# Optimization experiments

Measured on AMD Instinct MI355X. Metric: run time of the kernel, lower is better.

The kernel has to match this reference:

```python
import jax, jax.numpy as jnp
import numpy as np
import math

T, N, P, H, E, S, R = 64, 1024, 256, 256, 512, 16, 16

def _sincos(n, d):
    pos = np.arange(n)[:, None].astype(np.float32)
    div = np.exp(np.arange(0, d, 2).astype(np.float32) * -(math.log(10000.0) / d))
    pe = np.zeros((n, d), np.float32)
    pe[:, 0::2] = np.sin(pos * div)
    pe[:, 1::2] = np.cos(pos * div)
    return jnp.asarray(pe)

def setup_inputs():
    key = jax.random.key(0)
    ks = iter(jax.random.split(key, 40))
    def w(shape, s=0.05):
        return jax.random.normal(next(ks), shape, jnp.float32) * s
    adj_seq = (jax.random.uniform(next(ks), (T, N, N)) < 0.05).astype(jnp.float32)
    return dict(
        adj_seq=adj_seq,
        pos_emb=_sincos(N, P),
        g1_Wm=w((P, H)), g1_bm=jnp.zeros((H,), jnp.float32),
        g1_Wq=w((H, H)), g1_Wk=w((H, H)), g1_gb=jnp.asarray(-1.0, jnp.float32),
        g1_Wu=w((P + H, H)), g1_bu=jnp.zeros((H,), jnp.float32),
        g1_lg=jnp.ones((H,), jnp.float32), g1_lb=jnp.zeros((H,), jnp.float32),
        g2_Wm=w((H, H)), g2_bm=jnp.zeros((H,), jnp.float32),
        g2_Wu=w((2 * H, H)), g2_bu=jnp.zeros((H,), jnp.float32),
        g2_lg=jnp.ones((H,), jnp.float32), g2_lb=jnp.zeros((H,), jnp.float32),
        m_lg=jnp.ones((H,), jnp.float32), m_lb=jnp.zeros((H,), jnp.float32),
        m_Win=w((H, 2 * E)), m_bin=jnp.zeros((2 * E,), jnp.float32),
        m_Wdelta=w((E, R)), m_bdelta=jnp.zeros((R,), jnp.float32),
        m_Wdt=w((R, E)), m_bdt=jnp.zeros((E,), jnp.float32),
        m_WB=w((E, S)), m_bB=jnp.zeros((S,), jnp.float32),
        m_WC=w((E, S)), m_bC=jnp.zeros((S,), jnp.float32),
        m_Alog=-jnp.exp(w((E, S), 0.1)),
        m_D=jnp.zeros((E,), jnp.float32),
        m_Wout=w((E, H)), m_bout=jnp.zeros((H,), jnp.float32),
    )

def _ln(x, g, b):
    mu = x.mean(-1, keepdims=True)
    v = ((x - mu) ** 2).mean(-1, keepdims=True)
    return (x - mu) / jnp.sqrt(v + 1e-5) * g + b

def reference(adj_seq, pos_emb, g1_Wm, g1_bm, g1_Wq, g1_Wk, g1_gb, g1_Wu, g1_bu,
              g1_lg, g1_lb, g2_Wm, g2_bm, g2_Wu, g2_bu, g2_lg, g2_lb,
              m_lg, m_lb, m_Win, m_bin, m_Wdelta, m_bdelta, m_Wdt, m_bdt,
              m_WB, m_bB, m_WC, m_bC, m_Alog, m_D, m_Wout, m_bout):
    scale = math.sqrt(H) * max(1.0, 1e-6)  # sqrt(d) * gate_temperature

    def encode(adj):  # adj: [N,N]
        msgs = pos_emb @ g1_Wm + g1_bm                 # [N,H]
        q = msgs @ g1_Wq
        k = msgs @ g1_Wk
        gates = jax.nn.sigmoid(q @ k.T / scale + g1_gb)
        agg = (gates * adj) @ msgs                     # gated aggregation
        x = _ln(jax.nn.relu(jnp.concatenate([pos_emb, agg], -1) @ g1_Wu + g1_bu), g1_lg, g1_lb)
        msgs2 = x @ g2_Wm + g2_bm
        agg2 = adj @ msgs2                             # ungated layer 2
        x = _ln(jax.nn.relu(jnp.concatenate([x, agg2], -1) @ g2_Wu + g2_bu), g2_lg, g2_lb)
        return x                                       # [N,H]

    seq = jax.vmap(encode)(adj_seq)                    # [T,N,H]
    x = seq.transpose(1, 0, 2)                         # [N,T,H] node-batched sequences

    # --- MambaBlock ---
    res = x
    xn = _ln(x, m_lg, m_lb)
    xp = xn @ m_Win + m_bin
    u, gate = jnp.split(xp, 2, axis=-1)                # [N,T,E] each
    u = jax.nn.silu(u)
    delta = jax.nn.softplus((u @ m_Wdelta + m_bdelta) @ m_Wdt + m_bdt)  # [N,T,E]
    Bm = u @ m_WB + m_bB                               # [N,T,S]
    Cm = u @ m_WC + m_bC                               # [N,T,S]
    A = -jnp.exp(m_Alog)                               # [E,S]

    def step(h, inp):
        u_t, d_t, B_t, C_t = inp                       # [N,E],[N,E],[N,S],[N,S]
        Ad = jnp.exp(d_t[:, :, None] * A[None])        # [N,E,S]
        h = Ad * h + d_t[:, :, None] * B_t[:, None, :] * u_t[:, :, None]
        y = jnp.einsum('ns,nes->ne', C_t, h)
        return h, y

    h0 = jnp.zeros((N, E, S), x.dtype)
    _, ys = jax.lax.scan(step, h0, (u.transpose(1, 0, 2), delta.transpose(1, 0, 2),
                                    Bm.transpose(1, 0, 2), Cm.transpose(1, 0, 2)))
    y = ys.transpose(1, 0, 2)                          # [N,T,E]
    y = (y + u * m_D) * jax.nn.silu(gate)
    out = y @ m_Wout + m_bout + res                    # [N,T,H]
    return out.transpose(1, 0, 2)                      # [T,N,H]
```

## Files before the change

kernel.cpp:

```cpp
#include <hip/hip_runtime.h>
#include <hip/hip_bf16.h>

typedef __hip_bfloat16 bf16;
typedef __attribute__((ext_vector_type(8))) short s16x8;
typedef __attribute__((ext_vector_type(4))) short s16x4;
typedef __attribute__((ext_vector_type(4))) float f32x4;

#define TT 64
#define NN_ 1024
#define EE 512

__device__ __forceinline__ float toF(float v) { return v; }
__device__ __forceinline__ float toF(bf16 v) { return __bfloat162float(v); }
__device__ __forceinline__ bf16 f2b(float v) { return __float2bfloat16(v); }

#if __has_builtin(__builtin_amdgcn_exp2f)
#define EXP2F(x) __builtin_amdgcn_exp2f(x)
#else
#define EXP2F(x) exp2f(x)
#endif
#if __has_builtin(__builtin_amdgcn_logf)
#define LOG2F(x) __builtin_amdgcn_logf(x)
#else
#define LOG2F(x) log2f(x)
#endif

enum { EPI_F32 = 0, EPI_SIG_F32 = 1, EPI_SIG_B16 = 2 };
enum { E_LN1 = 0, E_BF16 = 1, E_LN2 = 2, E_SILU = 3, E_OUT = 4, E_TRI = 5, E_BF16T = 6 };

template <bool TRANSB, int EPI>
__global__ __launch_bounds__(256) void gemm_k(
    const float* __restrict__ A, const float* __restrict__ B,
    float* __restrict__ outF, const float* __restrict__ bias,
    const float* __restrict__ sbeta, float alpha,
    int M, int Nn, int K, int lda, int ldb)
{
    __shared__ float As[16][68];
    __shared__ float Bs[16][68];
    const int tid = threadIdx.x;
    const int tx = tid & 15, ty = tid >> 4;
    const int m0 = blockIdx.x * 64, n0 = blockIdx.y * 64;
    float acc[4][4] = {};

    for (int k0 = 0; k0 < K; k0 += 16) {
        {
            int row = tid >> 2, kk0 = (tid & 3) * 4, grow = m0 + row;
#pragma unroll
            for (int j = 0; j < 4; j++) {
                int kk = kk0 + j, gk = k0 + kk;
                As[kk][row] = (grow < M) ? A[(size_t)grow * lda + gk] : 0.f;
            }
        }
        if (!TRANSB) {
            int kk = tid >> 4, c0 = (tid & 15) * 4;
#pragma unroll
            for (int j = 0; j < 4; j++) {
                int col = c0 + j, gn = n0 + col;
                Bs[kk][col] = (gn < Nn) ? B[(size_t)(k0 + kk) * ldb + gn] : 0.f;
            }
        } else {
            int col = tid >> 2, kk0 = (tid & 3) * 4, gn = n0 + col;
#pragma unroll
            for (int j = 0; j < 4; j++) {
                int kk = kk0 + j;
                Bs[kk][col] = (gn < Nn) ? B[(size_t)gn * ldb + (k0 + kk)] : 0.f;
            }
        }
        __syncthreads();
#pragma unroll
        for (int kk = 0; kk < 16; kk++) {
            float a[4], b[4];
#pragma unroll
            for (int i = 0; i < 4; i++) a[i] = As[kk][ty * 4 + i];
#pragma unroll
            for (int j = 0; j < 4; j++) b[j] = Bs[kk][tx * 4 + j];
#pragma unroll
            for (int i = 0; i < 4; i++)
#pragma unroll
                for (int j = 0; j < 4; j++)
                    acc[i][j] = fmaf(a[i], b[j], acc[i][j]);
        }
        __syncthreads();
    }

    float gb = (EPI != EPI_F32 && sbeta) ? sbeta[0] : 0.f;
#pragma unroll
    for (int i = 0; i < 4; i++) {
        int row = m0 + ty * 4 + i;
        if (row >= M) continue;
#pragma unroll
        for (int j = 0; j < 4; j++) {
            int col = n0 + tx * 4 + j;
            if (col >= Nn) continue;
            float v = acc[i][j];
            if (EPI == EPI_F32) {
                if (bias) v += bias[col];
                outF[(size_t)row * Nn + col] = v;
            } else if (EPI == EPI_SIG_F32) {
                v = v * alpha + gb;
                outF[(size_t)row * Nn + col] = 1.f / (1.f + __expf(-v));
            } else {
                v = v * alpha + gb;
                ((bf16*)outF)[(size_t)row * Nn + col] = f2b(1.f / (1.f + __expf(-v)));
            }
        }
    }
}

template <int BM, int BN, bool CAT, int EPI>
__global__ __launch_bounds__(256) void mfma_k(
    const bf16* __restrict__ A1, const bf16* __restrict__ A2, unsigned rowmask,
    const bf16* __restrict__ BT, const float* __restrict__ bias,
    float* __restrict__ outF,
    bf16* __restrict__ outB, bf16* __restrict__ outB2,
    const float* __restrict__ g1, const float* __restrict__ b1,
    const float* __restrict__ g2, const float* __restrict__ b2,
    const bf16* __restrict__ resid,
    int M, int K)
{
    constexpr bool LN = (EPI == E_LN1 || EPI == E_LN2);
    constexpr int STAGE_B = (BM * 32 + BN * 32) * 2;
    constexpr int TRB = (EPI == E_BF16T) ? (64 * 268 * 2) : 0;
    constexpr int SB = LN ? (64 * 260 * 4) : (STAGE_B > TRB ? STAGE_B : TRB);
    __shared__ __align__(16) char smem[SB];
    short* As = (short*)smem;
    short* Bs = As + BM * 32;
    float* Cs = (float*)smem;

    const int tid = threadIdx.x;
    const int wid = tid >> 6, lane = tid & 63;
    const int wr = (BN == 256) ? 0 : wid;
    const int wc = (BN == 256) ? wid : 0;
    const int m0 = blockIdx.x * BM, n0 = blockIdx.y * BN;
    const int srow = tid >> 2;
    const int skoff = (tid & 3) * 8;

    f32x4 acc[4][4] = {};
    s16x8 pa[BM / 64], pbv[BN / 64];

    auto LOADT = [&](int k0) {
#pragma unroll
        for (int c = 0; c < BM / 64; c++) {
            int r = c * 64 + srow;
            int gr = m0 + r;
            const bf16* p;
            if (CAT) {
                int gk = k0 + skoff;
                p = (gk < 256) ? (A1 + (size_t)(gr & rowmask) * 256 + gk)
                               : (A2 + (size_t)gr * 256 + (gk - 256));
            } else {
                p = A1 + (size_t)gr * K + k0 + skoff;
            }
            pa[c] = *(const s16x8*)p;
        }
#pragma unroll
        for (int c = 0; c < BN / 64; c++) {
            int r = c * 64 + srow;
            pbv[c] = *(const s16x8*)(BT + (size_t)(n0 + r) * K + k0 + skoff);
        }
    };

    LOADT(0);
#pragma unroll 1
    for (int k0 = 0; k0 < K; k0 += 32) {
#pragma unroll
        for (int c = 0; c < BM / 64; c++)
            *(s16x8*)&As[(c * 64 + srow) * 32 + skoff] = pa[c];
#pragma unroll
        for (int c = 0; c < BN / 64; c++)
            *(s16x8*)&Bs[(c * 64 + srow) * 32 + skoff] = pbv[c];
        __syncthreads();
        if (k0 + 32 < K) LOADT(k0 + 32);
        s16x8 af[4], bf[4];
#pragma unroll
        for (int mi = 0; mi < 4; mi++)
            af[mi] = *(s16x8*)&As[(wr * 64 + mi * 16 + (lane & 15)) * 32 + (lane >> 4) * 8];
#pragma unroll
        for (int ni = 0; ni < 4; ni++)
            bf[ni] = *(s16x8*)&Bs[(wc * 64 + ni * 16 + (lane & 15)) * 32 + (lane >> 4) * 8];
#pragma unroll
        for (int mi = 0; mi < 4; mi++)
#pragma unroll
            for (int ni = 0; ni < 4; ni++)
                acc[mi][ni] = __builtin_amdgcn_mfma_f32_16x16x32_bf16(
                    af[mi], bf[ni], acc[mi][ni], 0, 0, 0);
        __syncthreads();
    }

    if (EPI == E_SILU) {
#pragma unroll
        for (int mi = 0; mi < 4; mi++)
#pragma unroll
            for (int ni = 0; ni < 4; ni++)
#pragma unroll
                for (int r = 0; r < 4; r++) {
                    int row = m0 + wr * 64 + mi * 16 + (lane >> 4) * 4 + r;
                    int col = n0 + wc * 64 + ni * 16 + (lane & 15);
                    float v = acc[mi][ni][r] + bias[col];
                    float s = v / (1.f + __expf(-v));
                    if (col < EE) outB[(size_t)row * EE + col] = f2b(s);
                    else          outB2[(size_t)row * EE + (col - EE)] = f2b(s);
                }
    } else if (EPI == E_BF16) {
#pragma unroll
        for (int mi = 0; mi < 4; mi++)
#pragma unroll
            for (int ni = 0; ni < 4; ni++)
#pragma unroll
                for (int r = 0; r < 4; r++) {
                    int row = m0 + wr * 64 + mi * 16 + (lane >> 4) * 4 + r;
                    int col = n0 + wc * 64 + ni * 16 + (lane & 15);
                    outB[(size_t)row * 256 + col] = f2b(acc[mi][ni][r] + bias[col]);
                }
    } else if (EPI == E_BF16T) {
        short* Ts = (short*)smem;
#pragma unroll
        for (int mi = 0; mi < 4; mi++)
#pragma unroll
            for (int ni = 0; ni < 4; ni++)
#pragma unroll
                for (int r = 0; r < 4; r++) {
                    int rl = mi * 16 + (lane >> 4) * 4 + r;
                    int cl = wc * 64 + ni * 16 + (lane & 15);
                    union { bf16 b; short s; } u;
                    u.b = f2b(acc[mi][ni][r] + bias[cl]);
                    Ts[rl * 268 + cl] = u.s;
                }
        __syncthreads();
        const int col = tid;
        size_t dbase = (((size_t)(m0 >> 10)) * 256 + col) * 1024 + (m0 & 1023);
#pragma unroll
        for (int j0 = 0; j0 < 64; j0 += 8) {
            s16x8 v;
#pragma unroll
            for (int i = 0; i < 8; i++) v[i] = Ts[(j0 + i) * 268 + col];
            *(s16x8*)&outB[dbase + j0] = v;
        }
    } else if (EPI == E_OUT) {
#pragma unroll
        for (int mi = 0; mi < 4; mi++)
#pragma unroll
            for (int ni = 0; ni < 4; ni++)
#pragma unroll
                for (int r = 0; r < 4; r++) {
                    int row = m0 + wr * 64 + mi * 16 + (lane >> 4) * 4 + r;
                    int col = n0 + wc * 64 + ni * 16 + (lane & 15);
                    float v = acc[mi][ni][r] + bias[col] + toF(resid[(size_t)row * 256 + col]);
                    int t = row & 63, n = row >> 6;
                    outF[((size_t)t * NN_ + n) * 256 + col] = v;
                }
    } else if (EPI == E_TRI) {
#pragma unroll
        for (int mi = 0; mi < 4; mi++)
#pragma unroll
            for (int ni = 0; ni < 4; ni++)
#pragma unroll
                for (int r = 0; r < 4; r++) {
                    int row = m0 + wid * 64 + mi * 16 + (lane >> 4) * 4 + r;
                    int col = ni * 16 + (lane & 15);
                    if (col < 48) {
                        float v = acc[mi][ni][r] + bias[col];
                        outF[(size_t)row * 48 + col] = v;
                    }
                }
    } else {
#pragma unroll
        for (int mi = 0; mi < 4; mi++)
#pragma unroll
            for (int ni = 0; ni < 4; ni++)
#pragma unroll
                for (int r = 0; r < 4; r++) {
                    int rl = mi * 16 + (lane >> 4) * 4 + r;
                    int cl = wc * 64 + ni * 16 + (lane & 15);
                    Cs[rl * 260 + cl] = fmaxf(acc[mi][ni][r] + bias[cl], 0.f);
                }
        __syncthreads();
        float g1v[4], b1v[4], g2v[4], b2v[4];
#pragma unroll
        for (int i = 0; i < 4; i++) {
            g1v[i] = g1[lane * 4 + i];
            b1v[i] = b1[lane * 4 + i];
            if (EPI == E_LN2) { g2v[i] = g2[lane * 4 + i]; b2v[i] = b2[lane * 4 + i]; }
        }
        for (int rr = 0; rr < 16; rr++) {
            int rl = wid * 16 + rr;
            int grow = m0 + rl;
            float x[4];
#pragma unroll
            for (int i = 0; i < 4; i++) x[i] = Cs[rl * 260 + lane * 4 + i];
            float s = x[0] + x[1] + x[2] + x[3];
#pragma unroll
            for (int o = 1; o < 64; o <<= 1) s += __shfl_xor(s, o, 64);
            float mu = s * (1.f / 256.f);
            float d[4], ss = 0.f;
#pragma unroll
            for (int i = 0; i < 4; i++) { d[i] = x[i] - mu; ss = fmaf(d[i], d[i], ss); }
#pragma unroll
            for (int o = 1; o < 64; o <<= 1) ss += __shfl_xor(ss, o, 64);
            float inv = rsqrtf(fmaxf(ss * (1.f / 256.f), 0.f) + 1e-5f);
            float y[4];
#pragma unroll
            for (int i = 0; i < 4; i++) y[i] = d[i] * inv * g1v[i] + b1v[i];
            if (EPI == E_LN1) {
                __align__(8) bf16 pk[4];
#pragma unroll
                for (int i = 0; i < 4; i++) pk[i] = f2b(y[i]);
                *(s16x4*)&outB[(size_t)grow * 256 + lane * 4] = *(s16x4*)pk;
            } else {
                int trow = (grow & 1023) * 64 + (grow >> 10);
                __align__(8) bf16 pk[4];
#pragma unroll
                for (int i = 0; i < 4; i++) pk[i] = f2b(y[i]);
                *(s16x4*)&outB[(size_t)trow * 256 + lane * 4] = *(s16x4*)pk;
                float s2 = y[0] + y[1] + y[2] + y[3];
#pragma unroll
                for (int o = 1; o < 64; o <<= 1) s2 += __shfl_xor(s2, o, 64);
                float mu2 = s2 * (1.f / 256.f);
                float d2[4], ss2 = 0.f;
#pragma unroll
                for (int i = 0; i < 4; i++) { d2[i] = y[i] - mu2; ss2 = fmaf(d2[i], d2[i], ss2); }
#pragma unroll
                for (int o = 1; o < 64; o <<= 1) ss2 += __shfl_xor(ss2, o, 64);
                float inv2 = rsqrtf(fmaxf(ss2 * (1.f / 256.f), 0.f) + 1e-5f);
                __align__(8) bf16 pk2[4];
#pragma unroll
                for (int i = 0; i < 4; i++) pk2[i] = f2b(d2[i] * inv2 * g2v[i] + b2v[i]);
                *(s16x4*)&outB2[(size_t)trow * 256 + lane * 4] = *(s16x4*)pk2;
            }
        }
    }
}

__global__ __launch_bounds__(256) void packadj_k(
    const float4* __restrict__ adj4, unsigned int* __restrict__ bits32)
{
    const size_t nwords = (size_t)TT * NN_ * NN_ / 32;
    const size_t stride = (size_t)gridDim.x * 256;
    for (size_t w = (size_t)blockIdx.x * 256 + threadIdx.x; w < nwords; w += stride) {
        const float4* __restrict__ p = adj4 + w * 8;
        float4 v[8];
#pragma unroll
        for (int i = 0; i < 8; i++) v[i] = p[i];
        unsigned int m = 0;
#pragma unroll
        for (int i = 0; i < 8; i++) {
            m |= (v[i].x != 0.f ? 1u : 0u) << (4 * i);
            m |= (v[i].y != 0.f ? 2u : 0u) << (4 * i);
            m |= (v[i].z != 0.f ? 4u : 0u) << (4 * i);
            m |= (v[i].w != 0.f ? 8u : 0u) << (4 * i);
        }
        bits32[w] = m;
    }
}

template <bool GATED>
__global__ __launch_bounds__(256, 2) void aggmm_k(
    const unsigned char* __restrict__ adjbits, const bf16* __restrict__ gatesb,
    const bf16* __restrict__ BTsrc, bf16* __restrict__ out)
{
    __shared__ __align__(16) short As[128 * 40];
    __shared__ __align__(16) short Bs[256 * 40];
    const int tid = threadIdx.x;
    const int wid = tid >> 6, lane = tid & 63;
    const int wr = wid & 1;
    const int wc = wid >> 1;
    const int bx = blockIdx.x;
    const int t = bx >> 3, n0 = (bx & 7) * 128;
    const int srow = tid >> 2;
    const int skoff = (tid & 3) * 8;

    const unsigned char* __restrict__ abB =
        adjbits + ((size_t)t * 1024 + n0) * 128 + (tid & 3);
    const bf16* __restrict__ gB = GATED ? (gatesb + (size_t)n0 * 1024 + skoff) : nullptr;
    const bf16* __restrict__ bt = GATED ? BTsrc : (BTsrc + (size_t)t * 256 * 1024);
    const size_t orow0 = (size_t)t * 1024 + n0;

    f32x4 acc[4][8] = {};

    unsigned char pm[2];
    s16x8 pg[2];
    s16x8 pb[4];

    auto LOADA = [&](int k0) {
#pragma unroll
        for (int c = 0; c < 2; c++) {
            int r = c * 64 + srow;
            pm[c] = abB[(size_t)r * 128 + (k0 >> 3)];
            if (GATED) pg[c] = *(const s16x8*)(gB + (size_t)r * 1024 + k0);
        }
#pragma unroll
        for (int c = 0; c < 4; c++)
            pb[c] = *(const s16x8*)(bt + (size_t)(c * 64 + srow) * 1024 + k0 + skoff);
    };
    auto STORE = [&]() {
#pragma unroll
        for (int c = 0; c < 2; c++) {
            unsigned m = pm[c];
            s16x8 tmp;
            if (GATED) {
#pragma unroll
                for (int i = 0; i < 8; i++) tmp[i] = ((m >> i) & 1) ? pg[c][i] : (short)0;
            } else {
#pragma unroll
                for (int i = 0; i < 8; i++) tmp[i] = ((m >> i) & 1) ? (short)0x3F80 : (short)0;
            }
            *(s16x8*)&As[(c * 64 + srow) * 40 + skoff] = tmp;
        }
#pragma unroll
        for (int c = 0; c < 4; c++)
            *(s16x8*)&Bs[(c * 64 + srow) * 40 + skoff] = pb[c];
    };

    LOADA(0);
#pragma unroll 1
    for (int k0 = 0; k0 < 1024; k0 += 32) {
        STORE();
        __syncthreads();
        if (k0 + 32 < 1024) LOADA(k0 + 32);
        s16x8 af[4];
#pragma unroll
        for (int mi = 0; mi < 4; mi++)
            af[mi] = *(s16x8*)&As[(wr * 64 + mi * 16 + (lane & 15)) * 40 + (lane >> 4) * 8];
#pragma unroll
        for (int ni = 0; ni < 8; ni++) {
            s16x8 bfv = *(s16x8*)&Bs[(wc * 128 + ni * 16 + (lane & 15)) * 40 + (lane >> 4) * 8];
#pragma unroll
            for (int mi = 0; mi < 4; mi++)
                acc[mi][ni] = __builtin_amdgcn_mfma_f32_16x16x32_bf16(
                    af[mi], bfv, acc[mi][ni], 0, 0, 0);
        }
        __syncthreads();
    }

#pragma unroll
    for (int mi = 0; mi < 4; mi++)
#pragma unroll
        for (int ni = 0; ni < 8; ni++)
#pragma unroll
            for (int r = 0; r < 4; r++) {
                int rowl = wr * 64 + mi * 16 + (lane >> 4) * 4 + r;
                int col = wc * 128 + ni * 16 + (lane & 15);
                out[(orow0 + rowl) * 256 + col] = f2b(acc[mi][ni][r]);
            }
}

__global__ __launch_bounds__(256) void scan_k(
    const bf16* __restrict__ u, const bf16* __restrict__ sg,
    const float* __restrict__ dbc,
    const float* __restrict__ Wdt, const float* __restrict__ bdt,
    const float* __restrict__ Alog, const float* __restrict__ D,
    bf16* __restrict__ yg)
{
    const int n = blockIdx.x, e = blockIdx.y * 256 + threadIdx.x;
    float al[16], wdt[16], h[16];
#pragma unroll
    for (int s = 0; s < 16; s++) {
        al[s] = -__expf(Alog[e * 16 + s]) * 1.44269504f;
        h[s] = 0.f;
    }
#pragma unroll
    for (int k = 0; k < 16; k++) wdt[k] = Wdt[(size_t)k * EE + e];
    const float bdte = bdt[e], De = D[e];
    const float* __restrict__ rowp = dbc + (size_t)n * TT * 48;
    const size_t base = (size_t)n * TT * EE + e;
#pragma unroll 2
    for (int t = 0; t < TT; t++) {
        const float* __restrict__ r = rowp + t * 48;
        float a0 = bdte, a1 = 0.f, a2 = 0.f, a3 = 0.f;
#pragma unroll
        for (int k = 0; k < 4; k++) {
            a0 = fmaf(r[k],      wdt[k],      a0);
            a1 = fmaf(r[k + 4],  wdt[k + 4],  a1);
            a2 = fmaf(r[k + 8],  wdt[k + 8],  a2);
            a3 = fmaf(r[k + 12], wdt[k + 12], a3);
        }
        float acc = (a0 + a1) + (a2 + a3);
        float delta = (acc > 20.f)
            ? acc
            : 0.69314718056f * LOG2F(1.f + EXP2F(acc * 1.44269504f));
        size_t idx = base + (size_t)t * EE;
        float uv = toF(u[idx]);
        float du = delta * uv;
        float y0 = 0.f, y1 = 0.f, y2 = 0.f, y3 = 0.f;
#pragma unroll
        for (int s = 0; s < 16; s += 4) {
            float ad0 = EXP2F(delta * al[s]);
            float ad1 = EXP2F(delta * al[s + 1]);
            float ad2 = EXP2F(delta * al[s + 2]);
            float ad3 = EXP2F(delta * al[s + 3]);
            h[s]     = fmaf(ad0, h[s],     du * r[16 + s]);
            h[s + 1] = fmaf(ad1, h[s + 1], du * r[17 + s]);
            h[s + 2] = fmaf(ad2, h[s + 2], du * r[18 + s]);
            h[s + 3] = fmaf(ad3, h[s + 3], du * r[19 + s]);
            y0 = fmaf(r[32 + s], h[s],     y0);
            y1 = fmaf(r[33 + s], h[s + 1], y1);
            y2 = fmaf(r[34 + s], h[s + 2], y2);
            y3 = fmaf(r[35 + s], h[s + 3], y3);
        }
        float y = (y0 + y1) + (y2 + y3);
        yg[idx] = f2b((y + uv * De) * toF(sg[idx]));
    }
}

__global__ void cast_k(const float* __restrict__ in, bf16* __restrict__ out, int n) {
    int i = blockIdx.x * 256 + threadIdx.x;
    if (i < n) out[i] = f2b(in[i]);
}
__global__ void transT_k(const float* __restrict__ W, bf16* __restrict__ out, int K, int Nn) {
    int gid = blockIdx.x * 256 + threadIdx.x;
    if (gid >= K * Nn) return;
    int n = gid / K, k = gid - n * K;
    out[gid] = f2b(W[(size_t)k * Nn + n]);
}
__global__ void transmsgs_k(const float* __restrict__ msgs, bf16* __restrict__ msgsT) {
    int gid = blockIdx.x * 256 + threadIdx.x;
    int c = gid >> 10, j = gid & 1023;
    msgsT[gid] = f2b(msgs[(size_t)j * 256 + c]);
}
__global__ void wdbct_k(const float* __restrict__ Wd, const float* __restrict__ WB,
                        const float* __restrict__ WC, bf16* __restrict__ out,
                        const float* __restrict__ bd, const float* __restrict__ bB,
                        const float* __restrict__ bC, float* __restrict__ biascat) {
    int gid = blockIdx.x * 256 + threadIdx.x;
    if (gid < 48) biascat[gid] = (gid < 16) ? bd[gid] : (gid < 32) ? bB[gid - 16] : bC[gid - 32];
    if (gid >= 64 * 512) return;
    int n = gid >> 9, k = gid & 511;
    float v = 0.f;
    if (n < 16)      v = Wd[(size_t)k * 16 + n];
    else if (n < 32) v = WB[(size_t)k * 16 + (n - 16)];
    else if (n < 48) v = WC[(size_t)k * 16 + (n - 32)];
    out[gid] = f2b(v);
}

extern "C" void kernel_launch(void* const* d_in, const int* in_sizes, int n_in,
                              void* d_out, int out_size, void* d_ws, size_t ws_size,
                              hipStream_t stream)
{
    const float* adj   = (const float*)d_in[0];
    const float* pos   = (const float*)d_in[1];
    const float* g1Wm  = (const float*)d_in[2];
    const float* g1bm  = (const float*)d_in[3];
    const float* g1Wq  = (const float*)d_in[4];
    const float* g1Wk  = (const float*)d_in[5];
    const float* g1gb  = (const float*)d_in[6];
    const float* g1Wu  = (const float*)d_in[7];
    const float* g1bu  = (const float*)d_in[8];
    const float* g1lg  = (const float*)d_in[9];
    const float* g1lb  = (const float*)d_in[10];
    const float* g2Wm  = (const float*)d_in[11];
    const float* g2bm  = (const float*)d_in[12];
    const float* g2Wu  = (const float*)d_in[13];
    const float* g2bu  = (const float*)d_in[14];
    const float* g2lg  = (const float*)d_in[15];
    const float* g2lb  = (const float*)d_in[16];
    const float* mlg   = (const float*)d_in[17];
    const float* mlb   = (const float*)d_in[18];
    const float* mWin  = (const float*)d_in[19];
    const float* mbin  = (const float*)d_in[20];
    const float* mWd   = (const float*)d_in[21];
    const float* mbd   = (const float*)d_in[22];
    const float* mWdt  = (const float*)d_in[23];
    const float* mbdt  = (const float*)d_in[24];
    const float* mWB   = (const float*)d_in[25];
    const float* mbB   = (const float*)d_in[26];
    const float* mWC   = (const float*)d_in[27];
    const float* mbC   = (const float*)d_in[28];
    const float* mAlog = (const float*)d_in[29];
    const float* mD    = (const float*)d_in[30];
    const float* mWout = (const float*)d_in[31];
    const float* mbout = (const float*)d_in[32];
    float* out = (float*)d_out;
    char* ws = (char*)d_ws;

    const size_t BIGE = (size_t)TT * NN_ * 256;
    size_t o = 0;
    auto alloc = [&](size_t bytes) { size_t r = o; o += (bytes + 255) & ~(size_t)255; return r; };

    float* msgs  = (float*)(ws + alloc((size_t)NN_ * 256 * 4));
    float* q     = (float*)(ws + alloc((size_t)NN_ * 256 * 4));
    float* kk    = (float*)(ws + alloc((size_t)NN_ * 256 * 4));
    bf16*  gatesb = (bf16*)(ws + alloc((size_t)NN_ * NN_ * 2));
    unsigned long long* adjbits =
        (unsigned long long*)(ws + alloc((size_t)TT * NN_ * NN_ / 8));
    bf16*  Ra    = (bf16*)(ws + alloc(BIGE * 2));
    size_t off_x1 = alloc(BIGE * 2);
    bf16*  x1    = (bf16*)(ws + off_x1);
    bf16*  agg2  = (bf16*)(ws + alloc(BIGE * 2));
    bf16*  x2    = (bf16*)(ws + alloc(BIGE * 2));
    bf16*  yg    = (bf16*)(ws + alloc(BIGE * 2));
    bf16*  sg    = (bf16*)(ws + alloc((size_t)NN_ * TT * EE * 2));
    float* dbc   = (float*)(ws + alloc((size_t)TT * NN_ * 48 * 4));
    bf16*  u     = (bf16*)(ws + off_x1);
    bf16* posb   = (bf16*)(ws + alloc((size_t)NN_ * 256 * 2));
    bf16* g1WuT  = (bf16*)(ws + alloc((size_t)256 * 512 * 2));
    bf16* g2WmT  = (bf16*)(ws + alloc((size_t)256 * 256 * 2));
    bf16* g2WuT  = (bf16*)(ws + alloc((size_t)256 * 512 * 2));
    bf16* mWinT  = (bf16*)(ws + alloc((size_t)1024 * 256 * 2));
    bf16* mWoutT = (bf16*)(ws + alloc((size_t)256 * 512 * 2));
    bf16* WdBCT  = (bf16*)(ws + alloc((size_t)64 * 512 * 2));
    float* biascat = (float*)(ws + alloc(64 * 4));
    bf16* msgsT  = (bf16*)(ws + alloc((size_t)256 * 1024 * 2));
    bf16* msgs2T = (bf16*)(ws + alloc(BIGE * 2));

    const unsigned ALLR = 0xFFFFFFFFu;
    const int M = TT * NN_;

    packadj_k<<<2048, 256, 0, stream>>>((const float4*)adj, (unsigned int*)adjbits);
    cast_k<<<NN_, 256, 0, stream>>>(pos, posb, NN_ * 256);
    transT_k<<<(512 * 256 + 255) / 256, 256, 0, stream>>>(g1Wu, g1WuT, 512, 256);
    transT_k<<<(256 * 256 + 255) / 256, 256, 0, stream>>>(g2Wm, g2WmT, 256, 256);
    transT_k<<<(512 * 256 + 255) / 256, 256, 0, stream>>>(g2Wu, g2WuT, 512, 256);
    transT_k<<<(256 * 1024 + 255) / 256, 256, 0, stream>>>(mWin, mWinT, 256, 1024);
    transT_k<<<(512 * 256 + 255) / 256, 256, 0, stream>>>(mWout, mWoutT, 512, 256);
    wdbct_k<<<(64 * 512 + 255) / 256, 256, 0, stream>>>(mWd, mWB, mWC, WdBCT, mbd, mbB, mbC, biascat);

    gemm_k<false, EPI_F32><<<dim3(16, 4), 256, 0, stream>>>(
        pos, g1Wm, msgs, g1bm, nullptr, 1.f, NN_, 256, 256, 256, 256);
    transmsgs_k<<<1024, 256, 0, stream>>>(msgs, msgsT);
    gemm_k<false, EPI_F32><<<dim3(16, 4), 256, 0, stream>>>(
        msgs, g1Wq, q, nullptr, nullptr, 1.f, NN_, 256, 256, 256, 256);
    gemm_k<false, EPI_F32><<<dim3(16, 4), 256, 0, stream>>>(
        msgs, g1Wk, kk, nullptr, nullptr, 1.f, NN_, 256, 256, 256, 256);
    gemm_k<true, EPI_SIG_B16><<<dim3(16, 16), 256, 0, stream>>>(
        q, kk, (float*)gatesb, nullptr, g1gb, 1.f / 16.f, NN_, NN_, 256, 256, 256);
    aggmm_k<true><<<512, 256, 0, stream>>>(
        (const unsigned char*)adjbits, gatesb, msgsT, Ra);
    mfma_k<64, 256, true, E_LN1><<<dim3(1024, 1), 256, 0, stream>>>(
        posb, Ra, 1023u, g1WuT, g1bu, nullptr, x1, nullptr,
        g1lg, g1lb, nullptr, nullptr, nullptr, M, 512);
    mfma_k<64, 256, false, E_BF16T><<<dim3(1024, 1), 256, 0, stream>>>(
        x1, x1, ALLR, g2WmT, g2bm, nullptr, msgs2T, nullptr,
        nullptr, nullptr, nullptr, nullptr, nullptr, M, 256);
    aggmm_k<false><<<512, 256, 0, stream>>>(
        (const unsigned char*)adjbits, nullptr, msgs2T, agg2);
    mfma_k<64, 256, true, E_LN2><<<dim3(1024, 1), 256, 0, stream>>>(
        x1, agg2, ALLR, g2WuT, g2bu, nullptr, x2, Ra,
        g2lg, g2lb, mlg, mlb, nullptr, M, 512);
    mfma_k<64, 256, false, E_SILU><<<dim3(1024, 4), 256, 0, stream>>>(
        Ra, Ra, ALLR, mWinT, mbin, nullptr, u, sg,
        nullptr, nullptr, nullptr, nullptr, nullptr, M, 256);
    mfma_k<256, 64, false, E_TRI><<<dim3(256, 1), 256, 0, stream>>>(
        u, u, ALLR, WdBCT, biascat, dbc, nullptr, nullptr,
        nullptr, nullptr, nullptr, nullptr, nullptr, M, 512);
    scan_k<<<dim3(NN_, 2), 256, 0, stream>>>(u, sg, dbc, mWdt, mbdt, mAlog, mD, yg);
    mfma_k<64, 256, false, E_OUT><<<dim3(1024, 1), 256, 0, stream>>>(
        yg, yg, ALLR, mWoutT, mbout, out, nullptr, nullptr,
        nullptr, nullptr, nullptr, nullptr, x2, M, 512);

    (void)in_sizes; (void)n_in; (void)out_size; (void)ws_size;
}
```

Measured before the change: 1.063 ms.

## Add 128x256-tile MFMA GEMM kernel with padded LDS for three plain-epilogue GEMMs

Introduces a new GEMM kernel with 128x256 block tiles, arranged as 2x2 waves each computing 64x128, and LDS rows padded to 40 elements to reduce bank conflicts. It replaces the 64x256 mfma_k launches for the g2 message projection, the Mamba input projection and the output projection, halving the grid in M. Each B fragment is now reused across four A fragments, raising arithmetic intensity per LDS read. The cost is more accumulator registers per thread (128 floats), bounded by launch_bounds(256,2), and a two-pass transposed-store epilogue.

```diff
diff --git a/kernel.cpp b/kernel.cpp
--- a/kernel.cpp
+++ b/kernel.cpp
@@ -120,8 +120,7 @@
 {
     constexpr bool LN = (EPI == E_LN1 || EPI == E_LN2);
     constexpr int STAGE_B = (BM * 32 + BN * 32) * 2;
-    constexpr int TRB = (EPI == E_BF16T) ? (64 * 268 * 2) : 0;
-    constexpr int SB = LN ? (64 * 260 * 4) : (STAGE_B > TRB ? STAGE_B : TRB);
+    constexpr int SB = LN ? (64 * 260 * 4) : STAGE_B;
     __shared__ __align__(16) char smem[SB];
     short* As = (short*)smem;
     short* Bs = As + BM * 32;
@@ -187,69 +186,7 @@
         __syncthreads();
     }
 
-    if (EPI == E_SILU) {
-#pragma unroll
-        for (int mi = 0; mi < 4; mi++)
-#pragma unroll
-            for (int ni = 0; ni < 4; ni++)
-#pragma unroll
-                for (int r = 0; r < 4; r++) {
-                    int row = m0 + wr * 64 + mi * 16 + (lane >> 4) * 4 + r;
-                    int col = n0 + wc * 64 + ni * 16 + (lane & 15);
-                    float v = acc[mi][ni][r] + bias[col];
-                    float s = v / (1.f + __expf(-v));
-                    if (col < EE) outB[(size_t)row * EE + col] = f2b(s);
-                    else          outB2[(size_t)row * EE + (col - EE)] = f2b(s);
-                }
-    } else if (EPI == E_BF16) {
-#pragma unroll
-        for (int mi = 0; mi < 4; mi++)
-#pragma unroll
-            for (int ni = 0; ni < 4; ni++)
-#pragma unroll
-                for (int r = 0; r < 4; r++) {
-                    int row = m0 + wr * 64 + mi * 16 + (lane >> 4) * 4 + r;
-                    int col = n0 + wc * 64 + ni * 16 + (lane & 15);
-                    outB[(size_t)row * 256 + col] = f2b(acc[mi][ni][r] + bias[col]);
-                }
-    } else if (EPI == E_BF16T) {
-        short* Ts = (short*)smem;
-#pragma unroll
-        for (int mi = 0; mi < 4; mi++)
-#pragma unroll
-            for (int ni = 0; ni < 4; ni++)
-#pragma unroll
-                for (int r = 0; r < 4; r++) {
-                    int rl = mi * 16 + (lane >> 4) * 4 + r;
-                    int cl = wc * 64 + ni * 16 + (lane & 15);
-                    union { bf16 b; short s; } u;
-                    u.b = f2b(acc[mi][ni][r] + bias[cl]);
-                    Ts[rl * 268 + cl] = u.s;
-                }
-        __syncthreads();
-        const int col = tid;
-        size_t dbase = (((size_t)(m0 >> 10)) * 256 + col) * 1024 + (m0 & 1023);
-#pragma unroll
-        for (int j0 = 0; j0 < 64; j0 += 8) {
-            s16x8 v;
-#pragma unroll
-            for (int i = 0; i < 8; i++) v[i] = Ts[(j0 + i) * 268 + col];
-            *(s16x8*)&outB[dbase + j0] = v;
-        }
-    } else if (EPI == E_OUT) {
-#pragma unroll
-        for (int mi = 0; mi < 4; mi++)
-#pragma unroll
-            for (int ni = 0; ni < 4; ni++)
-#pragma unroll
-                for (int r = 0; r < 4; r++) {
-                    int row = m0 + wr * 64 + mi * 16 + (lane >> 4) * 4 + r;
-                    int col = n0 + wc * 64 + ni * 16 + (lane & 15);
-                    float v = acc[mi][ni][r] + bias[col] + toF(resid[(size_t)row * 256 + col]);
-                    int t = row & 63, n = row >> 6;
-                    outF[((size_t)t * NN_ + n) * 256 + col] = v;
-                }
-    } else if (EPI == E_TRI) {
+    if (EPI == E_TRI) {
 #pragma unroll
         for (int mi = 0; mi < 4; mi++)
 #pragma unroll
@@ -326,6 +263,128 @@
 #pragma unroll
                 for (int i = 0; i < 4; i++) pk2[i] = f2b(d2[i] * inv2 * g2v[i] + b2v[i]);
                 *(s16x4*)&outB2[(size_t)trow * 256 + lane * 4] = *(s16x4*)pk2;
+            }
+        }
+    }
+}
+
+template <int EPI>
+__global__ __launch_bounds__(256, 2) void mfma2_k(
+    const bf16* __restrict__ A, const bf16* __restrict__ BT,
+    const float* __restrict__ bias,
+    float* __restrict__ outF, bf16* __restrict__ outB, bf16* __restrict__ outB2,
+    const bf16* __restrict__ resid,
+    int K)
+{
+    constexpr int STAGE_B = (128 * 40 + 256 * 40) * 2;
+    constexpr int TRB = (EPI == E_BF16T) ? (64 * 268 * 2) : 0;
+    constexpr int SB = STAGE_B > TRB ? STAGE_B : TRB;
+    __shared__ __align__(16) char smem[SB];
+    short* As = (short*)smem;
+    short* Bs = As + 128 * 40;
+
+    const int tid = threadIdx.x;
+    const int wid = tid >> 6, lane = tid & 63;
+    const int wr = wid & 1;
+    const int wc = wid >> 1;
+    const int m0 = blockIdx.x * 128, n0 = blockIdx.y * 256;
+    const int srow = tid >> 2;
+    const int skoff = (tid & 3) * 8;
+
+    f32x4 acc[4][8] = {};
+    s16x8 pa[2], pb[4];
+
+    auto LOADT = [&](int k0) {
+#pragma unroll
+        for (int c = 0; c < 2; c++)
+            pa[c] = *(const s16x8*)(A + (size_t)(m0 + c * 64 + srow) * K + k0 + skoff);
+#pragma unroll
+        for (int c = 0; c < 4; c++)
+            pb[c] = *(const s16x8*)(BT + (size_t)(n0 + c * 64 + srow) * K + k0 + skoff);
+    };
+
+    LOADT(0);
+#pragma unroll 1
+    for (int k0 = 0; k0 < K; k0 += 32) {
+#pragma unroll
+        for (int c = 0; c < 2; c++)
+            *(s16x8*)&As[(c * 64 + srow) * 40 + skoff] = pa[c];
+#pragma unroll
+        for (int c = 0; c < 4; c++)
+            *(s16x8*)&Bs[(c * 64 + srow) * 40 + skoff] = pb[c];
+        __syncthreads();
+        if (k0 + 32 < K) LOADT(k0 + 32);
+        s16x8 af[4];
+#pragma unroll
+        for (int mi = 0; mi < 4; mi++)
+            af[mi] = *(s16x8*)&As[(wr * 64 + mi * 16 + (lane & 15)) * 40 + (lane >> 4) * 8];
+#pragma unroll
+        for (int ni = 0; ni < 8; ni++) {
+            s16x8 bfv = *(s16x8*)&Bs[(wc * 128 + ni * 16 + (lane & 15)) * 40 + (lane >> 4) * 8];
+#pragma unroll
+            for (int mi = 0; mi < 4; mi++)
+                acc[mi][ni] = __builtin_amdgcn_mfma_f32_16x16x32_bf16(
+                    af[mi], bfv, acc[mi][ni], 0, 0, 0);
+        }
+        __syncthreads();
+    }
+
+    if (EPI == E_SILU) {
+#pragma unroll
+        for (int mi = 0; mi < 4; mi++)
+#pragma unroll
+            for (int ni = 0; ni < 8; ni++)
+#pragma unroll
+                for (int r = 0; r < 4; r++) {
+                    int row = m0 + wr * 64 + mi * 16 + (lane >> 4) * 4 + r;
+                    int col = n0 + wc * 128 + ni * 16 + (lane & 15);
+                    float v = acc[mi][ni][r] + bias[col];
+                    float s = v / (1.f + __expf(-v));
+                    if (col < EE) outB[(size_t)row * EE + col] = f2b(s);
+                    else          outB2[(size_t)row * EE + (col - EE)] = f2b(s);
+                }
+    } else if (EPI == E_OUT) {
+#pragma unroll
+        for (int mi = 0; mi < 4; mi++)
+#pragma unroll
+            for (int ni = 0; ni < 8; ni++)
+#pragma unroll
+                for (int r = 0; r < 4; r++) {
+                    int row = m0 + wr * 64 + mi * 16 + (lane >> 4) * 4 + r;
+                    int col = n0 + wc * 128 + ni * 16 + (lane & 15);
+                    float v = acc[mi][ni][r] + bias[col] + toF(resid[(size_t)row * 256 + col]);
+                    int t = row & 63, n = row >> 6;
+                    outF[((size_t)t * NN_ + n) * 256 + col] = v;
+                }
+    } else {
+        short* Ts = (short*)smem;
+#pragma unroll 1
+        for (int h = 0; h < 2; h++) {
+            if (h) __syncthreads();
+            if (wr == h) {
+#pragma unroll
+                for (int mi = 0; mi < 4; mi++)
+#pragma unroll
+                    for (int ni = 0; ni < 8; ni++)
+#pragma unroll
+                        for (int r = 0; r < 4; r++) {
+                            int rl = mi * 16 + (lane >> 4) * 4 + r;
+                            int cl = wc * 128 + ni * 16 + (lane & 15);
+                            union { bf16 b; short s; } u;
+                            u.b = f2b(acc[mi][ni][r] + bias[n0 + cl]);
+                            Ts[rl * 268 + cl] = u.s;
+                        }
+            }
+            __syncthreads();
+            const int col = tid;
+            const int rowbase = m0 + h * 64;
+            size_t dbase = (((size_t)(rowbase >> 10)) * 256 + (n0 + col)) * 1024 + (rowbase & 1023);
+#pragma unroll
+            for (int j0 = 0; j0 < 64; j0 += 8) {
+                s16x8 v;
+#pragma unroll
+                for (int i = 0; i < 8; i++) v[i] = Ts[(j0 + i) * 268 + col];
+                *(s16x8*)&outB[dbase + j0] = v;
             }
         }
     }
@@ -628,24 +687,21 @@
     mfma_k<64, 256, true, E_LN1><<<dim3(1024, 1), 256, 0, stream>>>(
         posb, Ra, 1023u, g1WuT, g1bu, nullptr, x1, nullptr,
         g1lg, g1lb, nullptr, nullptr, nullptr, M, 512);
-    mfma_k<64, 256, false, E_BF16T><<<dim3(1024, 1), 256, 0, stream>>>(
-        x1, x1, ALLR, g2WmT, g2bm, nullptr, msgs2T, nullptr,
-        nullptr, nullptr, nullptr, nullptr, nullptr, M, 256);
+    mfma2_k<E_BF16T><<<dim3(512, 1), 256, 0, stream>>>(
+        x1, g2WmT, g2bm, nullptr, msgs2T, nullptr, nullptr, 256);
     aggmm_k<false><<<512, 256, 0, stream>>>(
         (const unsigned char*)adjbits, nullptr, msgs2T, agg2);
     mfma_k<64, 256, true, E_LN2><<<dim3(1024, 1), 256, 0, stream>>>(
         x1, agg2, ALLR, g2WuT, g2bu, nullptr, x2, Ra,
         g2lg, g2lb, mlg, mlb, nullptr, M, 512);
-    mfma_k<64, 256, false, E_SILU><<<dim3(1024, 4), 256, 0, stream>>>(
-        Ra, Ra, ALLR, mWinT, mbin, nullptr, u, sg,
-        nullptr, nullptr, nullptr, nullptr, nullptr, M, 256);
+    mfma2_k<E_SILU><<<dim3(512, 4), 256, 0, stream>>>(
+        Ra, mWinT, mbin, nullptr, u, sg, nullptr, 256);
     mfma_k<256, 64, false, E_TRI><<<dim3(256, 1), 256, 0, stream>>>(
         u, u, ALLR, WdBCT, biascat, dbc, nullptr, nullptr,
         nullptr, nullptr, nullptr, nullptr, nullptr, M, 512);
     scan_k<<<dim3(NN_, 2), 256, 0, stream>>>(u, sg, dbc, mWdt, mbdt, mAlog, mD, yg);
-    mfma_k<64, 256, false, E_OUT><<<dim3(1024, 1), 256, 0, stream>>>(
-        yg, yg, ALLR, mWoutT, mbout, out, nullptr, nullptr,
-        nullptr, nullptr, nullptr, nullptr, x2, M, 512);
+    mfma2_k<E_OUT><<<dim3(512, 1), 256, 0, stream>>>(
+        yg, mWoutT, mbout, out, nullptr, nullptr, x2, 512);
 
     (void)in_sizes; (void)n_in; (void)out_size; (void)ws_size;
 }
```

After: 1.066 ms. No clear change (+0.3%).
